# Optimization experiments

Measured on AMD Instinct MI355X. Metric: run time of the kernel, lower is better.

## Reference

```python
import math
import jax, jax.numpy as jnp
import numpy as np

VOCAB = 80; MAX_SEQ_LEN = 32; D_MODEL = 512; NHEAD = 8; DFF = 2048; NLAYERS = 6
EOS = 1; SOS = 2; PAD = 0; BATCH = 8; MEM_LEN = 256; PE_LEN = MAX_SEQ_LEN + 2
EPS = 1e-5


def _sinusoid(max_len, d):
    pos = np.arange(max_len)[:, None].astype(np.float32)
    div = np.exp(np.arange(0, d, 2).astype(np.float32) * -(math.log(10000.0) / d))
    pe = np.zeros((max_len, d), np.float32)
    pe[:, 0::2] = np.sin(pos * div)
    pe[:, 1::2] = np.cos(pos * div)
    return jnp.asarray(pe)


def setup_inputs() -> dict:
    key = jax.random.key(0)
    ks = jax.random.split(key, 10)
    s = 0.02
    def n(k, shape, scale=s):
        return jax.random.normal(k, shape, jnp.float32) * scale
    return {
        "memory": n(ks[0], (BATCH, MEM_LEN, D_MODEL), 1.0),
        "emb_table": n(ks[1], (VOCAB, D_MODEL), 1.0),
        "pe": _sinusoid(PE_LEN, D_MODEL),
        "sa_in_w": n(ks[2], (NLAYERS, 3 * D_MODEL, D_MODEL)),
        "sa_in_b": jnp.zeros((NLAYERS, 3 * D_MODEL), jnp.float32),
        "sa_out_w": n(ks[3], (NLAYERS, D_MODEL, D_MODEL)),
        "sa_out_b": jnp.zeros((NLAYERS, D_MODEL), jnp.float32),
        "ca_in_w": n(ks[4], (NLAYERS, 3 * D_MODEL, D_MODEL)),
        "ca_in_b": jnp.zeros((NLAYERS, 3 * D_MODEL), jnp.float32),
        "ca_out_w": n(ks[5], (NLAYERS, D_MODEL, D_MODEL)),
        "ca_out_b": jnp.zeros((NLAYERS, D_MODEL), jnp.float32),
        "ln_w": jnp.ones((NLAYERS, 3, D_MODEL), jnp.float32),
        "ln_b": jnp.zeros((NLAYERS, 3, D_MODEL), jnp.float32),
        "ff1_w": n(ks[6], (NLAYERS, DFF, D_MODEL)),
        "ff1_b": jnp.zeros((NLAYERS, DFF), jnp.float32),
        "ff2_w": n(ks[7], (NLAYERS, D_MODEL, DFF)),
        "ff2_b": jnp.zeros((NLAYERS, D_MODEL), jnp.float32),
        "clf_w": n(ks[8], (VOCAB, D_MODEL)),
        "clf_b": jnp.zeros((VOCAB,), jnp.float32),
    }


def _layer_norm(x, g, b):
    mu = jnp.mean(x, -1, keepdims=True)
    var = jnp.mean((x - mu) ** 2, -1, keepdims=True)
    return (x - mu) * jax.lax.rsqrt(var + EPS) * g + b


def _mha(q_in, kv_in, in_w, in_b, out_w, out_b, mask):
    d = q_in.shape[-1]; hd = d // NHEAD
    wq, wk, wv = jnp.split(in_w, 3, 0)
    bq, bk, bv = jnp.split(in_b, 3)
    B, Tq, _ = q_in.shape; Tk = kv_in.shape[1]
    q = (q_in @ wq.T + bq).reshape(B, Tq, NHEAD, hd)
    k = (kv_in @ wk.T + bk).reshape(B, Tk, NHEAD, hd)
    v = (kv_in @ wv.T + bv).reshape(B, Tk, NHEAD, hd)
    scores = jnp.einsum('bqhd,bkhd->bhqk', q, k) / math.sqrt(hd)
    if mask is not None:
        scores = jnp.where(mask, -1e9, scores)
    probs = jax.nn.softmax(scores, -1)
    out = jnp.einsum('bhqk,bkhd->bqhd', probs, v).reshape(B, Tq, d)
    return out @ out_w.T + out_b


def _decoder(tgt, memory, causal, p):
    # post-norm TransformerDecoder (torch default, dropout=identity at inference)
    x = tgt
    for l in range(NLAYERS):
        x = _layer_norm(x + _mha(x, x, p['sa_in_w'][l], p['sa_in_b'][l], p['sa_out_w'][l], p['sa_out_b'][l], causal), p['ln_w'][l, 0], p['ln_b'][l, 0])
        x = _layer_norm(x + _mha(x, memory, p['ca_in_w'][l], p['ca_in_b'][l], p['ca_out_w'][l], p['ca_out_b'][l], None), p['ln_w'][l, 1], p['ln_b'][l, 1])
        h = jax.nn.gelu(x @ p['ff1_w'][l].T + p['ff1_b'][l], approximate=False)
        x = _layer_norm(x + h @ p['ff2_w'][l].T + p['ff2_b'][l], p['ln_w'][l, 2], p['ln_b'][l, 2])
    return x


def _greedy(memory, emb_table, pe, p, clf_w, clf_b):
    B = memory.shape[0]; T1 = MAX_SEQ_LEN + 1
    sq = math.sqrt(D_MODEL)
    causal = jnp.triu(jnp.ones((T1, T1), bool), 1)[None, None]  # True = blocked
    tgt0 = jnp.zeros((B, T1, D_MODEL), memory.dtype)
    tgt0 = tgt0.at[:, 0].set(pe[0] + emb_table[SOS] * sq)

    def step(tgt, t):
        # full recompute of the whole decoder stack each step (no KV cache),
        # causal mask makes position t depend only on the valid prefix.
        out = _decoder(tgt, memory, causal, p)
        out_t = jax.lax.dynamic_slice_in_dim(out, t, 1, 1)[:, 0]
        logits = out_t @ clf_w.T + clf_b
        pred = jnp.argmax(logits, -1)
        # original uses pe[len(sampled_ids)] == pe[t+2] for the token at slot t+1
        new_e = jnp.take(pe, t + 2, axis=0) + emb_table[pred] * sq
        tgt = jax.lax.dynamic_update_slice_in_dim(tgt, new_e[:, None, :], t + 1, 1)
        return tgt, (logits, pred)

    _, (logits, preds) = jax.lax.scan(step, tgt0, jnp.arange(MAX_SEQ_LEN))
    all_logits = jnp.transpose(logits, (1, 0, 2))  # [B, T, V]
    sampled = jnp.concatenate([jnp.full((B, 1), SOS, preds.dtype), preds.T], 1)
    eos_idx = jnp.argmax(sampled == EOS, 1)  # first eos (0 if none, as torch)
    sampled = jnp.where(jnp.arange(T1)[None] <= eos_idx[:, None], PAD, sampled)
    return all_logits, sampled


def reference(memory, emb_table, pe, sa_in_w, sa_in_b, sa_out_w, sa_out_b, ca_in_w, ca_in_b, ca_out_w, ca_out_b, ln_w, ln_b, ff1_w, ff1_b, ff2_w, ff2_b, clf_w, clf_b):
    p = dict(sa_in_w=sa_in_w, sa_in_b=sa_in_b, sa_out_w=sa_out_w, sa_out_b=sa_out_b,
             ca_in_w=ca_in_w, ca_in_b=ca_in_b, ca_out_w=ca_out_w, ca_out_b=ca_out_b,
             ln_w=ln_w, ln_b=ln_b, ff1_w=ff1_w, ff1_b=ff1_b, ff2_w=ff2_w, ff2_b=ff2_b)
    return _greedy(memory, emb_table, pe, p, clf_w, clf_b)
```

## Files before the change

kernel.cpp:

```cpp
#include <hip/hip_runtime.h>
#include <math.h>

constexpr int T1 = 33, NL = 6, VOC = 80;
constexpr float SQD = 22.62741699796952f;

__device__ float g_memk[(size_t)NL * 2048 * 512];
__device__ float g_memv[(size_t)NL * 2048 * 512];
__device__ float g_kc[(size_t)NL * 8 * T1 * 512];
__device__ float g_vc[(size_t)NL * 8 * T1 * 512];
__device__ float g_x[8 * 512], g_x2[8 * 512], g_y[8 * 512], g_q[8 * 512], g_att[8 * 512];
__device__ float g_h[8 * 2048];
__device__ int   g_tok[8 * T1];

struct DecP {
  const float *mem, *emb, *pe, *saw, *sab, *sow, *sob, *caw, *cab, *cow, *cob,
              *lnw, *lnb, *f1w, *f1b, *f2w, *f2b, *cw, *cb;
  float* out;
};

__global__ __launch_bounds__(256) void k_memkv(const float* __restrict__ mem,
                                               const float* __restrict__ caw,
                                               const float* __restrict__ cab) {
  __shared__ float mlds[128][34];
  __shared__ float wlds[256][34];
  const int tid = threadIdx.x;
  const int l = blockIdx.x / 64, rem = blockIdx.x % 64;
  const int mt = rem >> 2, rt = rem & 3;
  const float* wbase = caw + (size_t)l * 1536 * 512 + (size_t)512 * 512;

  float acc[8][16];
#pragma unroll
  for (int i = 0; i < 8; ++i)
#pragma unroll
    for (int j = 0; j < 16; ++j) acc[i][j] = 0.f;

  const int tm = tid >> 4, tr = tid & 15;

  for (int kb = 0; kb < 16; ++kb) {
    __syncthreads();
    {
      int row = tid >> 1, half = tid & 1;
      const float2* src = (const float2*)(mem + (size_t)(mt * 128 + row) * 512 + kb * 32 + half * 16);
      float2* dst = (float2*)&mlds[row][half * 16];
#pragma unroll
      for (int q = 0; q < 8; ++q) dst[q] = src[q];
    }
    {
      int c2 = (tid & 15) * 2, rb = tid >> 4;
#pragma unroll
      for (int q = 0; q < 16; ++q) {
        int row = rb + 16 * q;
        *(float2*)&wlds[row][c2] =
            *(const float2*)(wbase + (size_t)(rt * 256 + row) * 512 + kb * 32 + c2);
      }
    }
    __syncthreads();
#pragma unroll 4
    for (int k2 = 0; k2 < 16; ++k2) {
      float2 mv[8];
#pragma unroll
      for (int i = 0; i < 8; ++i) mv[i] = *(const float2*)&mlds[tm * 8 + i][2 * k2];
#pragma unroll
      for (int j = 0; j < 16; ++j) {
        float2 w2 = *(const float2*)&wlds[tr + 16 * j][2 * k2];
#pragma unroll
        for (int i = 0; i < 8; ++i) acc[i][j] += mv[i].x * w2.x + mv[i].y * w2.y;
      }
    }
  }
#pragma unroll
  for (int i = 0; i < 8; ++i) {
    int mrow = mt * 128 + tm * 8 + i;
#pragma unroll
    for (int j = 0; j < 16; ++j) {
      int r = rt * 256 + tr + 16 * j;
      float v = acc[i][j] + cab[l * 1536 + 512 + r];
      if (r < 512) g_memk[((size_t)l * 2048 + mrow) * 512 + r] = v;
      else         g_memv[((size_t)l * 2048 + mrow) * 512 + (r - 512)] = v;
    }
  }
}

__device__ __forceinline__ float wave_reduce8(const float (&acc)[8], int lane) {
  float a0, a1, a2, a3;
  {
    bool hi = lane & 1;
    float s0 = hi ? acc[0] : acc[1], s1 = hi ? acc[2] : acc[3];
    float s2 = hi ? acc[4] : acc[5], s3 = hi ? acc[6] : acc[7];
    float r0 = __shfl_xor(s0, 1), r1 = __shfl_xor(s1, 1);
    float r2 = __shfl_xor(s2, 1), r3 = __shfl_xor(s3, 1);
    a0 = (hi ? acc[1] : acc[0]) + r0;  a1 = (hi ? acc[3] : acc[2]) + r1;
    a2 = (hi ? acc[5] : acc[4]) + r2;  a3 = (hi ? acc[7] : acc[6]) + r3;
  }
  float b0, b1;
  {
    bool hi = lane & 2;
    float s0 = hi ? a0 : a1, s1 = hi ? a2 : a3;
    float r0 = __shfl_xor(s0, 2), r1 = __shfl_xor(s1, 2);
    b0 = (hi ? a1 : a0) + r0;  b1 = (hi ? a3 : a2) + r1;
  }
  float f;
  {
    bool hi = lane & 4;
    float s = hi ? b0 : b1;
    float r = __shfl_xor(s, 4);
    f = (hi ? b1 : b0) + r;
  }
  f += __shfl_xor(f, 8);  f += __shfl_xor(f, 16);  f += __shfl_xor(f, 32);
  return f;
}

__device__ __forceinline__ void keep8(const float (&w)[8]) {
  asm volatile("" :: "v"(w[0]), "v"(w[1]), "v"(w[2]), "v"(w[3]),
                     "v"(w[4]), "v"(w[5]), "v"(w[6]), "v"(w[7]));
}

__device__ __forceinline__ void stage512(float (*sx)[520], const float* __restrict__ g,
                                         bool doLN, const float* __restrict__ lw,
                                         const float* __restrict__ lb, float* __restrict__ wb) {
  const int tid = threadIdx.x;
#pragma unroll
  for (int q = 0; q < 2; ++q) {
    int f4 = tid + 512 * q;
    int b = f4 >> 7, c = (f4 & 127) << 2;
    float4 v = ((const float4*)g)[f4];
    *(float4*)&sx[b][c] = v;
  }
  __syncthreads();
  if (doLN) {
    const int lane = tid & 63, b = tid >> 6;
    float vals[8]; float sm = 0.f;
#pragma unroll
    for (int j = 0; j < 8; ++j) { vals[j] = sx[b][lane + 64 * j]; sm += vals[j]; }
#pragma unroll
    for (int o = 32; o; o >>= 1) sm += __shfl_xor(sm, o);
    float mu = sm * (1.f / 512.f);
    float s2 = 0.f;
#pragma unroll
    for (int j = 0; j < 8; ++j) { float d = vals[j] - mu; s2 += d * d; }
#pragma unroll
    for (int o = 32; o; o >>= 1) s2 += __shfl_xor(s2, o);
    float rstd = 1.f / sqrtf(s2 * (1.f / 512.f) + 1e-5f);
#pragma unroll
    for (int j = 0; j < 8; ++j) {
      int c = lane + 64 * j;
      sx[b][c] = (vals[j] - mu) * rstd * lw[c] + lb[c];
    }
    __syncthreads();
  }
  if (wb && blockIdx.x == 0) {
#pragma unroll
    for (int q = 0; q < 2; ++q) {
      int f4 = tid + 512 * q;
      int b = f4 >> 7, c = (f4 & 127) << 2;
      ((float4*)wb)[f4] = *(float4*)&sx[b][c];
    }
  }
}

template <int MODE>
__device__ __forceinline__ void gemv_pf(float (*sx)[520], const float (&w)[8], int r,
                                        const float* __restrict__ bias,
                                        float* __restrict__ out, const float* __restrict__ res,
                                        int l, int t) {
  const int lane = threadIdx.x & 63;
  float acc[8] = {0, 0, 0, 0, 0, 0, 0, 0};
#pragma unroll
  for (int j = 0; j < 8; ++j) {
#pragma unroll
    for (int b = 0; b < 8; ++b) acc[b] += w[j] * sx[b][lane + 64 * j];
  }
  float f = wave_reduce8(acc, lane);
  if (lane < 8) {
    const int b = lane;
    float v = f + bias[r];
    if constexpr (MODE == 0) {
      if (r < 512)       out[b * 512 + r] = v;
      else if (r < 1024) g_kc[(((size_t)l * 8 + b) * T1 + t) * 512 + (r - 512)] = v;
      else               g_vc[(((size_t)l * 8 + b) * T1 + t) * 512 + (r - 1024)] = v;
    } else if constexpr (MODE == 1) {
      out[b * 512 + r] = v + res[b * 512 + r];
    } else if constexpr (MODE == 2) {
      out[b * 512 + r] = v;
    } else {
      out[b * 2048 + r] = 0.5f * v * (1.f + erff(v * 0.70710678118654752f));
    }
  }
}

__global__ __launch_bounds__(256) void k_start(DecP P) {
  int b = blockIdx.x;
#pragma unroll
  for (int q = 0; q < 2; ++q) {
    int c = threadIdx.x + 256 * q;
    g_x[b * 512 + c] = P.pe[c] + P.emb[2 * 512 + c] * SQD;
  }
  if (threadIdx.x == 0) g_tok[b * T1] = 2;
}

__global__ __launch_bounds__(512) void k_A(DecP P, int l, int t) {
  __shared__ float sx[8][520];
  const int lane = threadIdx.x & 63, wv = threadIdx.x >> 6;
  const int r = blockIdx.x * 8 + wv;
  const float* wr = P.saw + (size_t)l * 1536 * 512 + (size_t)r * 512;
  float w[8];
#pragma unroll
  for (int j = 0; j < 8; ++j) w[j] = wr[lane + 64 * j];
  keep8(w);
  const float* lw = (l > 0) ? P.lnw + ((l - 1) * 3 + 2) * 512 : P.lnw;
  const float* lb = (l > 0) ? P.lnb + ((l - 1) * 3 + 2) * 512 : P.lnb;
  stage512(sx, (l == 0) ? g_x : g_y, l > 0, lw, lb, (l > 0) ? g_x : nullptr);
  gemv_pf<0>(sx, w, r, P.sab + l * 1536, g_q, nullptr, l, t);
}

__global__ __launch_bounds__(64) void k_B(DecP P, int l, int t) {
  __shared__ float s_p[128];
  const int lane = threadIdx.x;
  const int b = blockIdx.x >> 3, h = blockIdx.x & 7;
  s_p[lane] = g_q[b * 512 + h * 64 + lane];
  asm volatile("s_waitcnt lgkmcnt(0)" ::: "memory");
  __builtin_amdgcn_sched_barrier(0);
  float sc = -3.4e38f;
  if (lane <= t) {
    const float4* kr = (const float4*)&g_kc[(((size_t)l * 8 + b) * T1 + lane) * 512 + h * 64];
    float s = 0.f;
#pragma unroll
    for (int d4 = 0; d4 < 16; ++d4) {
      float4 kv = kr[d4];
      s += s_p[d4 * 4 + 0] * kv.x + s_p[d4 * 4 + 1] * kv.y +
           s_p[d4 * 4 + 2] * kv.z + s_p[d4 * 4 + 3] * kv.w;
    }
    sc = s * 0.125f;
  }
  float m = sc;
#pragma unroll
  for (int o = 32; o; o >>= 1) m = fmaxf(m, __shfl_xor(m, o));
  float ex = (lane <= t) ? expf(sc - m) : 0.f;
  float sum = ex;
#pragma unroll
  for (int o = 32; o; o >>= 1) sum += __shfl_xor(sum, o);
  s_p[64 + lane] = ex / sum;
  asm volatile("s_waitcnt lgkmcnt(0)" ::: "memory");
  __builtin_amdgcn_sched_barrier(0);
  float o = 0.f;
  for (int j = 0; j <= t; ++j)
    o += s_p[64 + j] * g_vc[(((size_t)l * 8 + b) * T1 + j) * 512 + h * 64 + lane];
  g_att[b * 512 + h * 64 + lane] = o;
}

__global__ __launch_bounds__(512) void k_C(DecP P, int l) {
  __shared__ float sx[8][520];
  const int lane = threadIdx.x & 63, wv = threadIdx.x >> 6;
  const int r = blockIdx.x * 8 + wv;
  const float* wr = P.sow + (size_t)l * 512 * 512 + (size_t)r * 512;
  float w[8];
#pragma unroll
  for (int j = 0; j < 8; ++j) w[j] = wr[lane + 64 * j];
  keep8(w);
  stage512(sx, g_att, false, nullptr, nullptr, nullptr);
  gemv_pf<1>(sx, w, r, P.sob + l * 512, g_y, g_x, l, 0);
}

__global__ __launch_bounds__(512) void k_D(DecP P, int l) {
  __shared__ float sx[8][520];
  const int lane = threadIdx.x & 63, wv = threadIdx.x >> 6;
  const int r = blockIdx.x * 8 + wv;
  const float* wr = P.caw + (size_t)l * 1536 * 512 + (size_t)r * 512;
  float w[8];
#pragma unroll
  for (int j = 0; j < 8; ++j) w[j] = wr[lane + 64 * j];
  keep8(w);
  stage512(sx, g_y, true, P.lnw + (l * 3 + 0) * 512, P.lnb + (l * 3 + 0) * 512, g_x2);
  gemv_pf<2>(sx, w, r, P.cab + l * 1536, g_q, nullptr, l, 0);
}

__global__ __launch_bounds__(256) void k_E(DecP P, int l) {
  __shared__ float s_p[336];
  __shared__ float s_w[4][2];
  __shared__ float s_pv[4][64];
  const int tid = threadIdx.x;
  const int lane = tid & 63, wv = tid >> 6;
  const int b = blockIdx.x >> 3, h = blockIdx.x & 7;
  if (tid < 64) s_p[tid] = g_q[b * 512 + h * 64 + tid];
  __syncthreads();
  int m0 = wv * 64 + lane;
  const float4* kr = (const float4*)&g_memk[((size_t)l * 2048 + b * 256 + m0) * 512 + h * 64];
  float s = 0.f;
#pragma unroll
  for (int d4 = 0; d4 < 16; ++d4) {
    float4 kv = kr[d4];
    s += s_p[d4 * 4 + 0] * kv.x + s_p[d4 * 4 + 1] * kv.y +
         s_p[d4 * 4 + 2] * kv.z + s_p[d4 * 4 + 3] * kv.w;
  }
  s *= 0.125f;
  float m = s;
#pragma unroll
  for (int o = 32; o; o >>= 1) m = fmaxf(m, __shfl_xor(m, o));
  if (lane == 0) s_w[wv][0] = m;
  __syncthreads();
  float M = fmaxf(fmaxf(s_w[0][0], s_w[1][0]), fmaxf(s_w[2][0], s_w[3][0]));
  float ex = expf(s - M);
  float sum = ex;
#pragma unroll
  for (int o = 32; o; o >>= 1) sum += __shfl_xor(sum, o);
  if (lane == 0) s_w[wv][1] = sum;
  __syncthreads();
  float S = s_w[0][1] + s_w[1][1] + s_w[2][1] + s_w[3][1];
  s_p[64 + m0] = ex / S;
  __syncthreads();
  float o = 0.f;
  const float* vbase = &g_memv[((size_t)l * 2048 + b * 256) * 512 + h * 64];
  for (int j = 0; j < 64; ++j) {
    int mm = wv * 64 + j;
    o += s_p[64 + mm] * vbase[(size_t)mm * 512 + lane];
  }
  s_pv[wv][lane] = o;
  __syncthreads();
  if (wv == 0) {
    float tot = s_pv[0][lane] + s_pv[1][lane] + s_pv[2][lane] + s_pv[3][lane];
    g_att[b * 512 + h * 64 + lane] = tot;
  }
}

__global__ __launch_bounds__(512) void k_F(DecP P, int l) {
  __shared__ float sx[8][520];
  const int lane = threadIdx.x & 63, wv = threadIdx.x >> 6;
  const int r = blockIdx.x * 8 + wv;
  const float* wr = P.cow + (size_t)l * 512 * 512 + (size_t)r * 512;
  float w[8];
#pragma unroll
  for (int j = 0; j < 8; ++j) w[j] = wr[lane + 64 * j];
  keep8(w);
  stage512(sx, g_att, false, nullptr, nullptr, nullptr);
  gemv_pf<1>(sx, w, r, P.cob + l * 512, g_y, g_x2, l, 0);
}

__global__ __launch_bounds__(512) void k_G(DecP P, int l) {
  __shared__ float sx[8][520];
  const int lane = threadIdx.x & 63, wv = threadIdx.x >> 6;
  const int r = blockIdx.x * 8 + wv;
  const float* wr = P.f1w + (size_t)l * 2048 * 512 + (size_t)r * 512;
  float w[8];
#pragma unroll
  for (int j = 0; j < 8; ++j) w[j] = wr[lane + 64 * j];
  keep8(w);
  stage512(sx, g_y, true, P.lnw + (l * 3 + 1) * 512, P.lnb + (l * 3 + 1) * 512, g_x2);
  gemv_pf<3>(sx, w, r, P.f1b + l * 2048, g_h, nullptr, l, 0);
}

__global__ __launch_bounds__(512) void k_H(DecP P, int l) {
  __shared__ float sb[8][2052];
  const int tid = threadIdx.x;
  const int lane = tid & 63, wv = tid >> 6;
  const int r = blockIdx.x * 8 + wv;
  const float* wr = P.f2w + (size_t)l * 512 * 2048 + (size_t)r * 2048;
  float w0[8], w1[8], w2[8], w3[8];
#pragma unroll
  for (int j = 0; j < 8; ++j) {
    w0[j] = wr[lane + 64 * j];
    w1[j] = wr[lane + 64 * (j + 8)];
    w2[j] = wr[lane + 64 * (j + 16)];
    w3[j] = wr[lane + 64 * (j + 24)];
  }
  keep8(w0); keep8(w1); keep8(w2); keep8(w3);
#pragma unroll
  for (int q = 0; q < 8; ++q) {
    int f4 = tid + 512 * q;
    int b = f4 >> 9, c = (f4 & 511) << 2;
    *(float4*)&sb[b][c] = ((const float4*)g_h)[f4];
  }
  __syncthreads();
  float acc[8] = {0, 0, 0, 0, 0, 0, 0, 0};
#pragma unroll
  for (int j = 0; j < 8; ++j) {
#pragma unroll
    for (int b = 0; b < 8; ++b) acc[b] += w0[j] * sb[b][lane + 64 * j];
  }
#pragma unroll
  for (int j = 0; j < 8; ++j) {
#pragma unroll
    for (int b = 0; b < 8; ++b) acc[b] += w1[j] * sb[b][lane + 64 * (j + 8)];
  }
#pragma unroll
  for (int j = 0; j < 8; ++j) {
#pragma unroll
    for (int b = 0; b < 8; ++b) acc[b] += w2[j] * sb[b][lane + 64 * (j + 16)];
  }
#pragma unroll
  for (int j = 0; j < 8; ++j) {
#pragma unroll
    for (int b = 0; b < 8; ++b) acc[b] += w3[j] * sb[b][lane + 64 * (j + 24)];
  }
  float f = wave_reduce8(acc, lane);
  if (lane < 8) g_y[lane * 512 + r] = f + P.f2b[l * 512 + r] + g_x2[lane * 512 + r];
}

__global__ __launch_bounds__(512) void k_T(DecP P, int t) {
  __shared__ float sx[8][520];
  __shared__ float s_p[80];
  __shared__ int s_int[1];
  const int tid = threadIdx.x;
  const int lane = tid & 63, wv = tid >> 6;
  const int b = blockIdx.x;
  stage512(sx, g_y, true, P.lnw + (5 * 3 + 2) * 512, P.lnb + (5 * 3 + 2) * 512, nullptr);
  for (int i = 0; i < 10; ++i) {
    int r = wv * 10 + i;
    const float* wr = P.cw + (size_t)r * 512;
    float a = 0.f;
#pragma unroll
    for (int j = 0; j < 8; ++j) a += wr[lane + 64 * j] * sx[b][lane + 64 * j];
#pragma unroll
    for (int o = 32; o; o >>= 1) a += __shfl_xor(a, o);
    if (lane == 0) {
      float v = a + P.cb[r];
      s_p[r] = v;
      P.out[((size_t)b * 32 + t) * VOC + r] = v;
    }
  }
  __syncthreads();
  if (wv == 0) {
    float v1 = s_p[lane];
    int i1 = lane;
    if (lane < 16) {
      float v2 = s_p[64 + lane];
      if (v2 > v1) { v1 = v2; i1 = 64 + lane; }
    }
#pragma unroll
    for (int o = 32; o; o >>= 1) {
      float ov = __shfl_xor(v1, o);
      int oi = __shfl_xor(i1, o);
      if (ov > v1 || (ov == v1 && oi < i1)) { v1 = ov; i1 = oi; }
    }
    if (lane == 0) { s_int[0] = i1; g_tok[b * T1 + t + 1] = i1; }
  }
  __syncthreads();
  int pred = s_int[0];
  {
    int c = tid;
    g_x[b * 512 + c] = P.pe[(t + 2) * 512 + c] + P.emb[(size_t)pred * 512 + c] * SQD;
  }
}

__global__ __launch_bounds__(64) void k_out(DecP P) {
  int lane = threadIdx.x;
  if (lane < 8) {
    int b = lane;
    int eos = -1;
    for (int j = 0; j < T1; ++j) {
      int tk = g_tok[b * T1 + j];
      if (tk == 1 && eos < 0) eos = j;
    }
    if (eos < 0) eos = 0;
    for (int j = 0; j < T1; ++j) {
      int tk = g_tok[b * T1 + j];
      P.out[20480 + b * T1 + j] = (j <= eos) ? 0.f : (float)tk;
    }
  }
}

extern "C" void kernel_launch(void* const* d_in, const int* in_sizes, int n_in,
                              void* d_out, int out_size, void* d_ws, size_t ws_size,
                              hipStream_t stream) {
  (void)in_sizes; (void)n_in; (void)d_ws; (void)ws_size; (void)out_size;
  const float* mem = (const float*)d_in[0];
  const float* emb = (const float*)d_in[1];
  const float* pe  = (const float*)d_in[2];
  const float* saw = (const float*)d_in[3];
  const float* sab = (const float*)d_in[4];
  const float* sow = (const float*)d_in[5];
  const float* sob = (const float*)d_in[6];
  const float* caw = (const float*)d_in[7];
  const float* cab = (const float*)d_in[8];
  const float* cow = (const float*)d_in[9];
  const float* cob = (const float*)d_in[10];
  const float* lnw = (const float*)d_in[11];
  const float* lnb = (const float*)d_in[12];
  const float* f1w = (const float*)d_in[13];
  const float* f1b = (const float*)d_in[14];
  const float* f2w = (const float*)d_in[15];
  const float* f2b = (const float*)d_in[16];
  const float* cw  = (const float*)d_in[17];
  const float* cb  = (const float*)d_in[18];

  DecP P{mem, emb, pe, saw, sab, sow, sob, caw, cab, cow, cob,
         lnw, lnb, f1w, f1b, f2w, f2b, cw, cb, (float*)d_out};

  hipLaunchKernelGGL(k_start, dim3(8), dim3(256), 0, stream, P);
  hipLaunchKernelGGL(k_memkv, dim3(384), dim3(256), 0, stream, mem, caw, cab);

  for (int t = 0; t < 32; ++t) {
    for (int l = 0; l < NL; ++l) {
      hipLaunchKernelGGL(k_A, dim3(192), dim3(512), 0, stream, P, l, t);
      hipLaunchKernelGGL(k_B, dim3(64), dim3(64), 0, stream, P, l, t);
      hipLaunchKernelGGL(k_C, dim3(64), dim3(512), 0, stream, P, l);
      hipLaunchKernelGGL(k_D, dim3(64), dim3(512), 0, stream, P, l);
      hipLaunchKernelGGL(k_E, dim3(64), dim3(256), 0, stream, P, l);
      hipLaunchKernelGGL(k_F, dim3(64), dim3(512), 0, stream, P, l);
      hipLaunchKernelGGL(k_G, dim3(256), dim3(512), 0, stream, P, l);
      hipLaunchKernelGGL(k_H, dim3(64), dim3(512), 0, stream, P, l);
    }
    hipLaunchKernelGGL(k_T, dim3(8), dim3(512), 0, stream, P, t);
  }
  hipLaunchKernelGGL(k_out, dim3(1), dim3(64), 0, stream, P);
}
```

Baseline: 8.023 ms.

## Fuse cross-attention LN and Q projection into attention kernel, head-major memory K/V

Removes the separate k_D kernel by computing the pre-cross-attention LayerNorm and the per-head query projection inside k_E, which now does all of its arithmetic in double precision. Memory K/V are re-laid out head-major so each block reads a contiguous 256x64 slice. All GEMV kernels move from 512-thread to 256-thread blocks with twice as many blocks. This saves one launch per layer per step but makes each attention block redo the LN and a 64-row projection, and the fp64 math is slow on this hardware.

Result: no change. 8.145 ms (+1.5%).

```diff
diff --git a/kernel.cpp b/kernel.cpp
--- a/kernel.cpp
+++ b/kernel.cpp
@@ -4,11 +4,11 @@
 constexpr int T1 = 33, NL = 6, VOC = 80;
 constexpr float SQD = 22.62741699796952f;
 
-__device__ float g_memk[(size_t)NL * 2048 * 512];
-__device__ float g_memv[(size_t)NL * 2048 * 512];
+__device__ float g_memk[(size_t)NL * 8 * 8 * 256 * 64];
+__device__ float g_memv[(size_t)NL * 8 * 8 * 256 * 64];
 __device__ float g_kc[(size_t)NL * 8 * T1 * 512];
 __device__ float g_vc[(size_t)NL * 8 * T1 * 512];
-__device__ float g_x[8 * 512], g_x2[8 * 512], g_y[8 * 512], g_q[8 * 512], g_att[8 * 512];
+__device__ float g_x[8 * 512], g_x2[8 * 512], g_x3[8 * 512], g_y[8 * 512], g_q[8 * 512], g_att[8 * 512];
 __device__ float g_h[8 * 2048];
 __device__ int   g_tok[8 * T1];
 
@@ -71,12 +71,18 @@
 #pragma unroll
   for (int i = 0; i < 8; ++i) {
     int mrow = mt * 128 + tm * 8 + i;
+    int bb = mrow >> 8, mm = mrow & 255;
 #pragma unroll
     for (int j = 0; j < 16; ++j) {
       int r = rt * 256 + tr + 16 * j;
       float v = acc[i][j] + cab[l * 1536 + 512 + r];
-      if (r < 512) g_memk[((size_t)l * 2048 + mrow) * 512 + r] = v;
-      else         g_memv[((size_t)l * 2048 + mrow) * 512 + (r - 512)] = v;
+      if (r < 512) {
+        int hh = r >> 6, d = r & 63;
+        g_memk[((((size_t)l * 8 + bb) * 8 + hh) * 256 + mm) * 64 + d] = v;
+      } else {
+        int r2 = r - 512, hh = r2 >> 6, d = r2 & 63;
+        g_memv[((((size_t)l * 8 + bb) * 8 + hh) * 256 + mm) * 64 + d] = v;
+      }
     }
   }
 }
@@ -110,48 +116,81 @@
   return f;
 }
 
+__device__ __forceinline__ double wave_reduce8d(const double (&acc)[8], int lane) {
+  double a0, a1, a2, a3;
+  {
+    bool hi = lane & 1;
+    double s0 = hi ? acc[0] : acc[1], s1 = hi ? acc[2] : acc[3];
+    double s2 = hi ? acc[4] : acc[5], s3 = hi ? acc[6] : acc[7];
+    double r0 = __shfl_xor(s0, 1), r1 = __shfl_xor(s1, 1);
+    double r2 = __shfl_xor(s2, 1), r3 = __shfl_xor(s3, 1);
+    a0 = (hi ? acc[1] : acc[0]) + r0;  a1 = (hi ? acc[3] : acc[2]) + r1;
+    a2 = (hi ? acc[5] : acc[4]) + r2;  a3 = (hi ? acc[7] : acc[6]) + r3;
+  }
+  double b0, b1;
+  {
+    bool hi = lane & 2;
+    double s0 = hi ? a0 : a1, s1 = hi ? a2 : a3;
+    double r0 = __shfl_xor(s0, 2), r1 = __shfl_xor(s1, 2);
+    b0 = (hi ? a1 : a0) + r0;  b1 = (hi ? a3 : a2) + r1;
+  }
+  double f;
+  {
+    bool hi = lane & 4;
+    double s = hi ? b0 : b1;
+    double r = __shfl_xor(s, 4);
+    f = (hi ? b1 : b0) + r;
+  }
+  f += __shfl_xor(f, 8);  f += __shfl_xor(f, 16);  f += __shfl_xor(f, 32);
+  return f;
+}
+
 __device__ __forceinline__ void keep8(const float (&w)[8]) {
   asm volatile("" :: "v"(w[0]), "v"(w[1]), "v"(w[2]), "v"(w[3]),
                      "v"(w[4]), "v"(w[5]), "v"(w[6]), "v"(w[7]));
 }
 
-__device__ __forceinline__ void stage512(float (*sx)[520], const float* __restrict__ g,
+__device__ __forceinline__ void stage_in(float (*sx)[520], const float* __restrict__ g,
                                          bool doLN, const float* __restrict__ lw,
                                          const float* __restrict__ lb, float* __restrict__ wb) {
   const int tid = threadIdx.x;
 #pragma unroll
-  for (int q = 0; q < 2; ++q) {
-    int f4 = tid + 512 * q;
+  for (int q = 0; q < 4; ++q) {
+    int f4 = tid + 256 * q;
     int b = f4 >> 7, c = (f4 & 127) << 2;
     float4 v = ((const float4*)g)[f4];
     *(float4*)&sx[b][c] = v;
   }
   __syncthreads();
   if (doLN) {
-    const int lane = tid & 63, b = tid >> 6;
-    float vals[8]; float sm = 0.f;
-#pragma unroll
-    for (int j = 0; j < 8; ++j) { vals[j] = sx[b][lane + 64 * j]; sm += vals[j]; }
-#pragma unroll
-    for (int o = 32; o; o >>= 1) sm += __shfl_xor(sm, o);
-    float mu = sm * (1.f / 512.f);
-    float s2 = 0.f;
-#pragma unroll
-    for (int j = 0; j < 8; ++j) { float d = vals[j] - mu; s2 += d * d; }
-#pragma unroll
-    for (int o = 32; o; o >>= 1) s2 += __shfl_xor(s2, o);
-    float rstd = 1.f / sqrtf(s2 * (1.f / 512.f) + 1e-5f);
-#pragma unroll
-    for (int j = 0; j < 8; ++j) {
-      int c = lane + 64 * j;
-      sx[b][c] = (vals[j] - mu) * rstd * lw[c] + lb[c];
+    const int lane = tid & 63, wv = tid >> 6;
+#pragma unroll
+    for (int rr = 0; rr < 2; ++rr) {
+      int b = wv + 4 * rr;
+      float vals[8]; float sm = 0.f;
+#pragma unroll
+      for (int j = 0; j < 8; ++j) { vals[j] = sx[b][lane + 64 * j]; sm += vals[j]; }
+#pragma unroll
+      for (int o = 32; o; o >>= 1) sm += __shfl_xor(sm, o);
+      float mu = sm * (1.f / 512.f);
+      float s2 = 0.f;
+#pragma unroll
+      for (int j = 0; j < 8; ++j) { float d = vals[j] - mu; s2 += d * d; }
+#pragma unroll
+      for (int o = 32; o; o >>= 1) s2 += __shfl_xor(s2, o);
+      float rstd = 1.f / sqrtf(s2 * (1.f / 512.f) + 1e-5f);
+#pragma unroll
+      for (int j = 0; j < 8; ++j) {
+        int c = lane + 64 * j;
+        sx[b][c] = (vals[j] - mu) * rstd * lw[c] + lb[c];
+      }
     }
     __syncthreads();
   }
   if (wb && blockIdx.x == 0) {
 #pragma unroll
-    for (int q = 0; q < 2; ++q) {
-      int f4 = tid + 512 * q;
+    for (int q = 0; q < 4; ++q) {
+      int f4 = tid + 256 * q;
       int b = f4 >> 7, c = (f4 & 127) << 2;
       ((float4*)wb)[f4] = *(float4*)&sx[b][c];
     }
@@ -180,8 +219,6 @@
       else               g_vc[(((size_t)l * 8 + b) * T1 + t) * 512 + (r - 1024)] = v;
     } else if constexpr (MODE == 1) {
       out[b * 512 + r] = v + res[b * 512 + r];
-    } else if constexpr (MODE == 2) {
-      out[b * 512 + r] = v;
     } else {
       out[b * 2048 + r] = 0.5f * v * (1.f + erff(v * 0.70710678118654752f));
     }
@@ -198,10 +235,10 @@
   if (threadIdx.x == 0) g_tok[b * T1] = 2;
 }
 
-__global__ __launch_bounds__(512) void k_A(DecP P, int l, int t) {
+__global__ __launch_bounds__(256) void k_A(DecP P, int l, int t) {
   __shared__ float sx[8][520];
   const int lane = threadIdx.x & 63, wv = threadIdx.x >> 6;
-  const int r = blockIdx.x * 8 + wv;
+  const int r = blockIdx.x * 4 + wv;
   const float* wr = P.saw + (size_t)l * 1536 * 512 + (size_t)r * 512;
   float w[8];
 #pragma unroll
@@ -209,7 +246,7 @@
   keep8(w);
   const float* lw = (l > 0) ? P.lnw + ((l - 1) * 3 + 2) * 512 : P.lnw;
   const float* lb = (l > 0) ? P.lnb + ((l - 1) * 3 + 2) * 512 : P.lnb;
-  stage512(sx, (l == 0) ? g_x : g_y, l > 0, lw, lb, (l > 0) ? g_x : nullptr);
+  stage_in(sx, (l == 0) ? g_x : g_y, l > 0, lw, lb, (l > 0) ? g_x : nullptr);
   gemv_pf<0>(sx, w, r, P.sab + l * 1536, g_q, nullptr, l, t);
 }
 
@@ -248,111 +285,146 @@
   g_att[b * 512 + h * 64 + lane] = o;
 }
 
-__global__ __launch_bounds__(512) void k_C(DecP P, int l) {
+__global__ __launch_bounds__(256) void k_C(DecP P, int l) {
   __shared__ float sx[8][520];
   const int lane = threadIdx.x & 63, wv = threadIdx.x >> 6;
-  const int r = blockIdx.x * 8 + wv;
+  const int r = blockIdx.x * 4 + wv;
   const float* wr = P.sow + (size_t)l * 512 * 512 + (size_t)r * 512;
   float w[8];
 #pragma unroll
   for (int j = 0; j < 8; ++j) w[j] = wr[lane + 64 * j];
   keep8(w);
-  stage512(sx, g_att, false, nullptr, nullptr, nullptr);
+  stage_in(sx, g_att, false, nullptr, nullptr, nullptr);
   gemv_pf<1>(sx, w, r, P.sob + l * 512, g_y, g_x, l, 0);
 }
 
-__global__ __launch_bounds__(512) void k_D(DecP P, int l) {
-  __shared__ float sx[8][520];
-  const int lane = threadIdx.x & 63, wv = threadIdx.x >> 6;
-  const int r = blockIdx.x * 8 + wv;
-  const float* wr = P.caw + (size_t)l * 1536 * 512 + (size_t)r * 512;
-  float w[8];
-#pragma unroll
-  for (int j = 0; j < 8; ++j) w[j] = wr[lane + 64 * j];
-  keep8(w);
-  stage512(sx, g_y, true, P.lnw + (l * 3 + 0) * 512, P.lnb + (l * 3 + 0) * 512, g_x2);
-  gemv_pf<2>(sx, w, r, P.cab + l * 1536, g_q, nullptr, l, 0);
-}
-
 __global__ __launch_bounds__(256) void k_E(DecP P, int l) {
-  __shared__ float s_p[336];
-  __shared__ float s_w[4][2];
-  __shared__ float s_pv[4][64];
+  __shared__ float s_x[512];
+  __shared__ float s_q[64];
+  __shared__ float s_att[64];
+  __shared__ float s_prob[256];
+  __shared__ double s_redd[8];
+  __shared__ double s_pvd[4][64];
+  __shared__ float s_mx[4];
   const int tid = threadIdx.x;
   const int lane = tid & 63, wv = tid >> 6;
   const int b = blockIdx.x >> 3, h = blockIdx.x & 7;
-  if (tid < 64) s_p[tid] = g_q[b * 512 + h * 64 + tid];
+
+  {
+    float2 yv = ((const float2*)(g_y + b * 512))[tid];
+    float v0 = yv.x, v1 = yv.y;
+    double sm = (double)v0 + (double)v1;
+    double sq = (double)v0 * (double)v0 + (double)v1 * (double)v1;
+#pragma unroll
+    for (int o = 32; o; o >>= 1) { sm += __shfl_xor(sm, o); sq += __shfl_xor(sq, o); }
+    if (lane == 0) { s_redd[wv] = sm; s_redd[4 + wv] = sq; }
+    __syncthreads();
+    double S = (s_redd[0] + s_redd[1]) + (s_redd[2] + s_redd[3]);
+    double Q = (s_redd[4] + s_redd[5]) + (s_redd[6] + s_redd[7]);
+    double mu = S * (1.0 / 512.0);
+    double var = Q * (1.0 / 512.0) - mu * mu;
+    double rstd = 1.0 / sqrt(var + 1e-5);
+    const float* lw = P.lnw + (l * 3 + 0) * 512;
+    const float* lb = P.lnb + (l * 3 + 0) * 512;
+    float f0 = (float)(((double)v0 - mu) * rstd * (double)lw[2 * tid] + (double)lb[2 * tid]);
+    float f1 = (float)(((double)v1 - mu) * rstd * (double)lw[2 * tid + 1] + (double)lb[2 * tid + 1]);
+    s_x[2 * tid] = f0; s_x[2 * tid + 1] = f1;
+    if (h == 0) { g_x2[b * 512 + 2 * tid] = f0; g_x2[b * 512 + 2 * tid + 1] = f1; }
+    __syncthreads();
+  }
+
+  {
+    const float* Wq = P.caw + (size_t)l * 1536 * 512 + (size_t)(h * 64) * 512;
+    const float* Bq = P.cab + l * 1536 + h * 64;
+#pragma unroll
+    for (int it = 0; it < 2; ++it) {
+      int d0 = it * 32 + wv * 8;
+      double acc[8];
+#pragma unroll
+      for (int i = 0; i < 8; ++i) {
+        const float* wr = Wq + (size_t)(d0 + i) * 512;
+        double a = 0.0;
+#pragma unroll
+        for (int j = 0; j < 8; ++j) a += (double)wr[lane + 64 * j] * (double)s_x[lane + 64 * j];
+        acc[i] = a;
+      }
+      double f = wave_reduce8d(acc, lane);
+      if (lane < 8) s_q[d0 + lane] = (float)(f + (double)Bq[d0 + lane]);
+    }
+  }
   __syncthreads();
-  int m0 = wv * 64 + lane;
-  const float4* kr = (const float4*)&g_memk[((size_t)l * 2048 + b * 256 + m0) * 512 + h * 64];
-  float s = 0.f;
-#pragma unroll
-  for (int d4 = 0; d4 < 16; ++d4) {
-    float4 kv = kr[d4];
-    s += s_p[d4 * 4 + 0] * kv.x + s_p[d4 * 4 + 1] * kv.y +
-         s_p[d4 * 4 + 2] * kv.z + s_p[d4 * 4 + 3] * kv.w;
-  }
-  s *= 0.125f;
-  float m = s;
-#pragma unroll
-  for (int o = 32; o; o >>= 1) m = fmaxf(m, __shfl_xor(m, o));
-  if (lane == 0) s_w[wv][0] = m;
-  __syncthreads();
-  float M = fmaxf(fmaxf(s_w[0][0], s_w[1][0]), fmaxf(s_w[2][0], s_w[3][0]));
-  float ex = expf(s - M);
-  float sum = ex;
-#pragma unroll
-  for (int o = 32; o; o >>= 1) sum += __shfl_xor(sum, o);
-  if (lane == 0) s_w[wv][1] = sum;
-  __syncthreads();
-  float S = s_w[0][1] + s_w[1][1] + s_w[2][1] + s_w[3][1];
-  s_p[64 + m0] = ex / S;
-  __syncthreads();
-  float o = 0.f;
-  const float* vbase = &g_memv[((size_t)l * 2048 + b * 256) * 512 + h * 64];
-  for (int j = 0; j < 64; ++j) {
-    int mm = wv * 64 + j;
-    o += s_p[64 + mm] * vbase[(size_t)mm * 512 + lane];
-  }
-  s_pv[wv][lane] = o;
-  __syncthreads();
-  if (wv == 0) {
-    float tot = s_pv[0][lane] + s_pv[1][lane] + s_pv[2][lane] + s_pv[3][lane];
-    g_att[b * 512 + h * 64 + lane] = tot;
-  }
-}
-
-__global__ __launch_bounds__(512) void k_F(DecP P, int l) {
+
+  {
+    size_t slice = (((size_t)l * 8 + b) * 8 + h) * 256;
+    int p = wv * 64 + lane;
+    const float4* kr = (const float4*)(g_memk + (slice + p) * 64);
+    double s = 0.0;
+#pragma unroll
+    for (int j = 0; j < 16; ++j) {
+      float4 kv = kr[j];
+      s += (double)s_q[4 * j] * (double)kv.x + (double)s_q[4 * j + 1] * (double)kv.y +
+           (double)s_q[4 * j + 2] * (double)kv.z + (double)s_q[4 * j + 3] * (double)kv.w;
+    }
+    float sc = (float)(s * 0.125);
+    float m = sc;
+#pragma unroll
+    for (int o = 32; o; o >>= 1) m = fmaxf(m, __shfl_xor(m, o));
+    if (lane == 0) s_mx[wv] = m;
+    __syncthreads();
+    float M = fmaxf(fmaxf(s_mx[0], s_mx[1]), fmaxf(s_mx[2], s_mx[3]));
+    double ex = exp((double)sc - (double)M);
+    double sum = ex;
+#pragma unroll
+    for (int o = 32; o; o >>= 1) sum += __shfl_xor(sum, o);
+    if (lane == 0) s_redd[4 + wv] = sum;
+    __syncthreads();
+    double S = (s_redd[4] + s_redd[5]) + (s_redd[6] + s_redd[7]);
+    s_prob[p] = (float)(ex / S);
+    __syncthreads();
+    double acc = 0.0;
+    const float* vb = g_memv + (slice + wv * 64) * 64 + lane;
+#pragma unroll 8
+    for (int j = 0; j < 64; ++j) acc += (double)s_prob[wv * 64 + j] * (double)vb[(size_t)j * 64];
+    s_pvd[wv][lane] = acc;
+    __syncthreads();
+    if (wv == 0) {
+      float av = (float)((s_pvd[0][lane] + s_pvd[1][lane]) + (s_pvd[2][lane] + s_pvd[3][lane]));
+      g_att[b * 512 + h * 64 + lane] = av;
+    }
+  }
+}
+
+__global__ __launch_bounds__(256) void k_F(DecP P, int l) {
   __shared__ float sx[8][520];
   const int lane = threadIdx.x & 63, wv = threadIdx.x >> 6;
-  const int r = blockIdx.x * 8 + wv;
+  const int r = blockIdx.x * 4 + wv;
   const float* wr = P.cow + (size_t)l * 512 * 512 + (size_t)r * 512;
   float w[8];
 #pragma unroll
   for (int j = 0; j < 8; ++j) w[j] = wr[lane + 64 * j];
   keep8(w);
-  stage512(sx, g_att, false, nullptr, nullptr, nullptr);
+  stage_in(sx, g_att, false, nullptr, nullptr, nullptr);
   gemv_pf<1>(sx, w, r, P.cob + l * 512, g_y, g_x2, l, 0);
 }
 
-__global__ __launch_bounds__(512) void k_G(DecP P, int l) {
+__global__ __launch_bounds__(256) void k_G(DecP P, int l) {
   __shared__ float sx[8][520];
   const int lane = threadIdx.x & 63, wv = threadIdx.x >> 6;
-  const int r = blockIdx.x * 8 + wv;
+  const int r = blockIdx.x * 4 + wv;
   const float* wr = P.f1w + (size_t)l * 2048 * 512 + (size_t)r * 512;
   float w[8];
 #pragma unroll
   for (int j = 0; j < 8; ++j) w[j] = wr[lane + 64 * j];
   keep8(w);
-  stage512(sx, g_y, true, P.lnw + (l * 3 + 1) * 512, P.lnb + (l * 3 + 1) * 512, g_x2);
+  stage_in(sx, g_y, true, P.lnw + (l * 3 + 1) * 512, P.lnb + (l * 3 + 1) * 512, g_x3);
   gemv_pf<3>(sx, w, r, P.f1b + l * 2048, g_h, nullptr, l, 0);
 }
 
-__global__ __launch_bounds__(512) void k_H(DecP P, int l) {
+__global__ __launch_bounds__(256) void k_H(DecP P, int l) {
   __shared__ float sb[8][2052];
   const int tid = threadIdx.x;
   const int lane = tid & 63, wv = tid >> 6;
-  const int r = blockIdx.x * 8 + wv;
+  const int r = blockIdx.x * 4 + wv;
   const float* wr = P.f2w + (size_t)l * 512 * 2048 + (size_t)r * 2048;
   float w0[8], w1[8], w2[8], w3[8];
 #pragma unroll
@@ -364,8 +436,8 @@
   }
   keep8(w0); keep8(w1); keep8(w2); keep8(w3);
 #pragma unroll
-  for (int q = 0; q < 8; ++q) {
-    int f4 = tid + 512 * q;
+  for (int q = 0; q < 16; ++q) {
+    int f4 = tid + 256 * q;
     int b = f4 >> 9, c = (f4 & 511) << 2;
     *(float4*)&sb[b][c] = ((const float4*)g_h)[f4];
   }
@@ -392,7 +464,7 @@
     for (int b = 0; b < 8; ++b) acc[b] += w3[j] * sb[b][lane + 64 * (j + 24)];
   }
   float f = wave_reduce8(acc, lane);
-  if (lane < 8) g_y[lane * 512 + r] = f + P.f2b[l * 512 + r] + g_x2[lane * 512 + r];
+  if (lane < 8) g_y[lane * 512 + r] = f + P.f2b[l * 512 + r] + g_x3[lane * 512 + r];
 }
 
 __global__ __launch_bounds__(512) void k_T(DecP P, int t) {
@@ -402,7 +474,37 @@
   const int tid = threadIdx.x;
   const int lane = tid & 63, wv = tid >> 6;
   const int b = blockIdx.x;
-  stage512(sx, g_y, true, P.lnw + (5 * 3 + 2) * 512, P.lnb + (5 * 3 + 2) * 512, nullptr);
+  {
+#pragma unroll
+    for (int q = 0; q < 2; ++q) {
+      int f4 = tid + 512 * q;
+      int bb = f4 >> 7, c = (f4 & 127) << 2;
+      float4 v = ((const float4*)g_y)[f4];
+      *(float4*)&sx[bb][c] = v;
+    }
+    __syncthreads();
+    const float* lw = P.lnw + (5 * 3 + 2) * 512;
+    const float* lb = P.lnb + (5 * 3 + 2) * 512;
+    int bb = tid >> 6;
+    float vals[8]; float sm = 0.f;
+#pragma unroll
+    for (int j = 0; j < 8; ++j) { vals[j] = sx[bb][lane + 64 * j]; sm += vals[j]; }
+#pragma unroll
+    for (int o = 32; o; o >>= 1) sm += __shfl_xor(sm, o);
+    float mu = sm * (1.f / 512.f);
+    float s2 = 0.f;
+#pragma unroll
+    for (int j = 0; j < 8; ++j) { float d = vals[j] - mu; s2 += d * d; }
+#pragma unroll
+    for (int o = 32; o; o >>= 1) s2 += __shfl_xor(s2, o);
+    float rstd = 1.f / sqrtf(s2 * (1.f / 512.f) + 1e-5f);
+#pragma unroll
+    for (int j = 0; j < 8; ++j) {
+      int c = lane + 64 * j;
+      sx[bb][c] = (vals[j] - mu) * rstd * lw[c] + lb[c];
+    }
+    __syncthreads();
+  }
   for (int i = 0; i < 10; ++i) {
     int r = wv * 10 + i;
     const float* wr = P.cw + (size_t)r * 512;
@@ -490,14 +592,13 @@
 
   for (int t = 0; t < 32; ++t) {
     for (int l = 0; l < NL; ++l) {
-      hipLaunchKernelGGL(k_A, dim3(192), dim3(512), 0, stream, P, l, t);
+      hipLaunchKernelGGL(k_A, dim3(384), dim3(256), 0, stream, P, l, t);
       hipLaunchKernelGGL(k_B, dim3(64), dim3(64), 0, stream, P, l, t);
-      hipLaunchKernelGGL(k_C, dim3(64), dim3(512), 0, stream, P, l);
-      hipLaunchKernelGGL(k_D, dim3(64), dim3(512), 0, stream, P, l);
+      hipLaunchKernelGGL(k_C, dim3(128), dim3(256), 0, stream, P, l);
       hipLaunchKernelGGL(k_E, dim3(64), dim3(256), 0, stream, P, l);
-      hipLaunchKernelGGL(k_F, dim3(64), dim3(512), 0, stream, P, l);
-      hipLaunchKernelGGL(k_G, dim3(256), dim3(512), 0, stream, P, l);
-      hipLaunchKernelGGL(k_H, dim3(64), dim3(512), 0, stream, P, l);
+      hipLaunchKernelGGL(k_F, dim3(128), dim3(256), 0, stream, P, l);
+      hipLaunchKernelGGL(k_G, dim3(512), dim3(256), 0, stream, P, l);
+      hipLaunchKernelGGL(k_H, dim3(128), dim3(256), 0, stream, P, l);
     }
     hipLaunchKernelGGL(k_T, dim3(8), dim3(512), 0, stream, P, t);
   }
```
